# Optimization experiments

Measured on AMD Instinct MI355X. Metric: run time of the kernel, lower is better.

Reference implementation:

```python
import jax, jax.numpy as jnp
import numpy as np

N, E = 100000, 1600000
IN_C, HID, OUT_C = 128, 16, 32
H1, H2 = 8, 8  # heads for conv1/conv2; conv3 has 1 head, concat=False
NEG_SLOPE = 0.2


def setup_inputs() -> dict:
    key = jax.random.key(0)
    ks = jax.random.split(key, 16)
    def p(k, shape, fan_in):
        return jax.random.normal(k, shape, jnp.float32) * (1.0 / np.sqrt(fan_in))
    inp = {
        "x": jax.random.normal(ks[0], (N, IN_C), jnp.float32),
        "edge_index": jax.random.randint(ks[1], (2, E), 0, N, jnp.int32),
        # conv1: in=128 -> heads=8, ch=16, concat
        "W1": p(ks[2], (IN_C, H1 * HID), IN_C),
        "a_src1": p(ks[3], (H1, HID), HID),
        "a_dst1": p(ks[4], (H1, HID), HID),
        "b1": jnp.zeros((H1 * HID,), jnp.float32),
        # conv2: in=128 -> heads=8, ch=16, concat
        "W2": p(ks[5], (H1 * HID, H2 * HID), H1 * HID),
        "a_src2": p(ks[6], (H2, HID), HID),
        "a_dst2": p(ks[7], (H2, HID), HID),
        "b2": jnp.zeros((H2 * HID,), jnp.float32),
        # conv3: in=128 -> heads=1, ch=32, concat=False
        "W3": p(ks[8], (H2 * HID, OUT_C), H2 * HID),
        "a_src3": p(ks[9], (1, OUT_C), OUT_C),
        "a_dst3": p(ks[10], (1, OUT_C), OUT_C),
        "b3": jnp.zeros((OUT_C,), jnp.float32),
    }
    return inp


def gat_conv(x, src, dst, W, a_src, a_dst, b, heads, ch, concat):
    """PyG-style GATConv (eval mode): gather -> leaky_relu -> segment softmax -> scatter sum."""
    n = x.shape[0]
    h = (x @ W).reshape(n, heads, ch)                 # [N, H, C]
    al_s = jnp.sum(h * a_src, axis=-1)                # [N, H] source-side logit part
    al_d = jnp.sum(h * a_dst, axis=-1)                # [N, H] dest-side logit part
    logits = jax.nn.leaky_relu(al_s[src] + al_d[dst], NEG_SLOPE)  # [Etot, H]
    m = jax.ops.segment_max(logits, dst, num_segments=n)         # per-dest max (self loops guarantee >=1 edge)
    e = jnp.exp(logits - m[dst])
    denom = jax.ops.segment_sum(e, dst, num_segments=n)
    alpha = e / denom[dst]                            # [Etot, H]
    msgs = h[src] * alpha[..., None]                  # [Etot, H, C]
    out = jax.ops.segment_sum(msgs, dst, num_segments=n)  # [N, H, C]
    if concat:
        return out.reshape(n, heads * ch) + b
    return out.mean(axis=1) + b


def reference(x, edge_index, W1, a_src1, a_dst1, b1, W2, a_src2, a_dst2, b2,
              W3, a_src3, a_dst3, b3):
    n = x.shape[0]
    loops = jnp.arange(n, dtype=edge_index.dtype)     # PyG add_self_loops=True
    src = jnp.concatenate([edge_index[0], loops])
    dst = jnp.concatenate([edge_index[1], loops])
    h = jax.nn.relu(gat_conv(x, src, dst, W1, a_src1, a_dst1, b1, H1, HID, True))
    h = jax.nn.relu(gat_conv(h, src, dst, W2, a_src2, a_dst2, b2, H2, HID, True))
    h = gat_conv(h, src, dst, W3, a_src3, a_dst3, b3, 1, OUT_C, False)
    # global_mean_pool with all-zero batch vector -> mean over all nodes
    return h.mean(axis=0, keepdims=True)              # [1, OUT_C]
```

## Files before the change

kernel.cpp:

```cpp
#include <hip/hip_runtime.h>


typedef unsigned short bfu;
typedef unsigned char u8;
typedef __attribute__((ext_vector_type(8))) short bf16x8;
typedef __attribute__((ext_vector_type(4))) float f32x4;
typedef __attribute__((ext_vector_type(2))) float f32x2;

constexpr int N_NODES = 100000;
constexpr int E_IN    = 1600000;
constexpr int E_TOT   = E_IN + N_NODES;
constexpr float NEG   = 0.2f;
constexpr int P_XCD   = 8;
constexpr int PSZ     = N_NODES / P_XCD;
constexpr int CAP     = 64;
constexpr int AGG32_B = N_NODES / 32;
constexpr int AGG128_B = N_NODES / 32;
constexpr int GEMM_B  = (N_NODES + 63) / 64;
constexpr int EDGE_B4 = (E_TOT / 4 + 255) / 256;
constexpr int FILL_B  = EDGE_B4 * P_XCD;
constexpr int PREP_ITEMS = 43008;
constexpr int PREP_B  = (PREP_ITEMS + 255) / 256;

__device__ inline bfu f2bf(float f) {
    union { float f; unsigned i; } c; c.f = f;
    unsigned x = c.i;
    return (bfu)((x + 0x7fffu + ((x >> 16) & 1u)) >> 16);
}
__device__ inline u8 f2fp8(float f) {
    return (u8)(__builtin_amdgcn_cvt_pk_fp8_f32(f, f, 0, false) & 0xff);
}


__device__ inline void prep_body(int idx,
        const float* __restrict__ W1, const float* __restrict__ W2,
        const float* __restrict__ W3,
        const float* __restrict__ as1, const float* __restrict__ ad1,
        const float* __restrict__ as2, const float* __restrict__ ad2,
        const float* __restrict__ as3, const float* __restrict__ ad3,
        bfu* __restrict__ WtX1, bfu* __restrict__ WtX2, bfu* __restrict__ WtX3) {
    if (idx < 16384) {
        int k = idx >> 7, n = idx & 127;
        WtX1[n * 128 + k] = f2bf(W1[idx]);
    } else if (idx < 32768) {
        int r = idx - 16384;
        int k = r >> 7, n = r & 127;
        WtX2[n * 128 + k] = f2bf(W2[r]);
    } else if (idx < 36864) {
        int r = idx - 32768;
        int k = r >> 5, n = r & 31;
        WtX3[n * 128 + k] = f2bf(W3[r]);
    } else if (idx < 38912) {
        int r = idx - 36864;
        int sd = r >> 10, rr = r & 1023;
        int h = rr >> 7, k = rr & 127;
        const float* a = sd ? ad1 : as1;
        float v = 0.f;
        #pragma unroll
        for (int c = 0; c < 16; ++c) v += W1[k * 128 + h * 16 + c] * a[h * 16 + c];
        WtX1[(128 + sd * 8 + h) * 128 + k] = f2bf(v);
    } else if (idx < 40960) {
        int r = idx - 38912;
        int sd = r >> 10, rr = r & 1023;
        int h = rr >> 7, k = rr & 127;
        const float* a = sd ? ad2 : as2;
        float v = 0.f;
        #pragma unroll
        for (int c = 0; c < 16; ++c) v += W2[k * 128 + h * 16 + c] * a[h * 16 + c];
        WtX2[(128 + sd * 8 + h) * 128 + k] = f2bf(v);
    } else if (idx < 41216) {
        int r = idx - 40960;
        int sd = r >> 7, k = r & 127;
        const float* a = sd ? ad3 : as3;
        float v = 0.f;
        #pragma unroll
        for (int c = 0; c < 32; ++c) v += W3[k * 32 + c] * a[c];
        WtX3[(32 + sd) * 128 + k] = f2bf(v);
    } else if (idx < 43008) {
        WtX3[34 * 128 + (idx - 41216)] = 0;
    }
}


__global__ __launch_bounds__(256) void fill_prep(const int* __restrict__ ei,
        int* __restrict__ cursor, int* __restrict__ srclist,
        const float* __restrict__ W1, const float* __restrict__ W2,
        const float* __restrict__ W3,
        const float* __restrict__ as1, const float* __restrict__ ad1,
        const float* __restrict__ as2, const float* __restrict__ ad2,
        const float* __restrict__ as3, const float* __restrict__ ad3,
        bfu* __restrict__ WtX1, bfu* __restrict__ WtX2, bfu* __restrict__ WtX3) {
    if (blockIdx.x >= FILL_B) {
        int idx = (blockIdx.x - FILL_B) * 256 + threadIdx.x;
        prep_body(idx, W1, W2, W3, as1, ad1, as2, ad2, as3, ad3, WtX1, WtX2, WtX3);
        return;
    }
    int p = blockIdx.x & 7;
    int b = blockIdx.x >> 3;
    int lo = p * PSZ, hi = lo + PSZ;
    int e0 = (b * 256 + threadIdx.x) * 4;
    if (e0 >= E_TOT) return;
    bool self = e0 >= E_IN;
    int4 d4;
    if (!self) d4 = *(const int4*)&ei[E_IN + e0];
    else { int bb = e0 - E_IN; d4 = make_int4(bb, bb + 1, bb + 2, bb + 3); }
    int dd[4] = {d4.x, d4.y, d4.z, d4.w};
    #pragma unroll
    for (int q = 0; q < 4; ++q) {
        int d = dd[q];
        if (d >= lo && d < hi) {
            int s = self ? (e0 - E_IN + q) : ei[e0 + q];
            int pos = atomicAdd(&cursor[d], 1);
            if (pos < CAP) srclist[d * CAP + pos] = s;
        }
    }
}


__device__ inline bf16x8 ldcvt_f32(const float* p) {
    float4 v0 = *(const float4*)p;
    float4 v1 = *(const float4*)(p + 4);
    bf16x8 a;
    a[0] = (short)f2bf(v0.x); a[1] = (short)f2bf(v0.y);
    a[2] = (short)f2bf(v0.z); a[3] = (short)f2bf(v0.w);
    a[4] = (short)f2bf(v1.x); a[5] = (short)f2bf(v1.y);
    a[6] = (short)f2bf(v1.z); a[7] = (short)f2bf(v1.w);
    return a;
}

template<int NTO, bool F32A>
__global__ __launch_bounds__(256) void gemm_mfma(const void* __restrict__ Xg_,
                                                 const bfu* __restrict__ Wt,
                                                 u8* __restrict__ Y,
                                                 float* __restrict__ als,
                                                 float* __restrict__ ald) {
    constexpr int COUT = NTO * 16;
    int wid  = threadIdx.x >> 6;
    int lane = threadIdx.x & 63;
    int m = lane & 15, quad = lane >> 4;
    int rbase = (blockIdx.x * 4 + wid) * 16;
    if (rbase >= N_NODES) return;
    int rA = rbase + m; if (rA >= N_NODES) rA = N_NODES - 1;

    bf16x8 a0, a1, a2, a3;
    if constexpr (F32A) {
        const float* Ap = (const float*)Xg_ + (size_t)rA * 128 + quad * 8;
        a0 = ldcvt_f32(Ap);
        a1 = ldcvt_f32(Ap + 32);
        a2 = ldcvt_f32(Ap + 64);
        a3 = ldcvt_f32(Ap + 96);
    } else {
        const bfu* Ap = (const bfu*)Xg_ + (size_t)rA * 128 + quad * 8;
        a0 = *(const bf16x8*)(Ap);
        a1 = *(const bf16x8*)(Ap + 32);
        a2 = *(const bf16x8*)(Ap + 64);
        a3 = *(const bf16x8*)(Ap + 96);
    }

    const bfu* Bp = Wt + (size_t)m * 128 + quad * 8;
    f32x4 acc[NTO + 1];
    #pragma unroll
    for (int nt = 0; nt <= NTO; nt++) {
        const bfu* Bn = Bp + nt * 16 * 128;
        f32x4 c = {0.f, 0.f, 0.f, 0.f};
        c = __builtin_amdgcn_mfma_f32_16x16x32_bf16(a0, *(const bf16x8*)(Bn),      c, 0, 0, 0);
        c = __builtin_amdgcn_mfma_f32_16x16x32_bf16(a1, *(const bf16x8*)(Bn + 32), c, 0, 0, 0);
        c = __builtin_amdgcn_mfma_f32_16x16x32_bf16(a2, *(const bf16x8*)(Bn + 64), c, 0, 0, 0);
        c = __builtin_amdgcn_mfma_f32_16x16x32_bf16(a3, *(const bf16x8*)(Bn + 96), c, 0, 0, 0);
        acc[nt] = c;
    }

    #pragma unroll
    for (int nt = 0; nt < NTO; nt++) {
        #pragma unroll
        for (int r = 0; r < 4; r++) {
            int row = rbase + quad * 4 + r;
            if (row < N_NODES)
                Y[(size_t)row * COUT + nt * 16 + m] = f2fp8(acc[nt][r]);
        }
    }
    #pragma unroll
    for (int r = 0; r < 4; r++) {
        int row = rbase + quad * 4 + r;
        if (row >= N_NODES) continue;
        float v = acc[NTO][r];
        if constexpr (NTO == 8) {
            if (m < 8) als[row * 8 + m] = v;
            else       ald[row * 8 + (m - 8)] = v;
        } else {
            if (m == 0) als[row] = v;
            else if (m == 1) ald[row] = v;
        }
    }
}


__device__ inline void unpack_fma(uint4 u, float w, float* a) {
    f32x2 p;
    p = __builtin_amdgcn_cvt_pk_f32_fp8((int)u.x, false); a[0]=fmaf(w,p[0],a[0]);  a[1]=fmaf(w,p[1],a[1]);
    p = __builtin_amdgcn_cvt_pk_f32_fp8((int)u.x, true);  a[2]=fmaf(w,p[0],a[2]);  a[3]=fmaf(w,p[1],a[3]);
    p = __builtin_amdgcn_cvt_pk_f32_fp8((int)u.y, false); a[4]=fmaf(w,p[0],a[4]);  a[5]=fmaf(w,p[1],a[5]);
    p = __builtin_amdgcn_cvt_pk_f32_fp8((int)u.y, true);  a[6]=fmaf(w,p[0],a[6]);  a[7]=fmaf(w,p[1],a[7]);
    p = __builtin_amdgcn_cvt_pk_f32_fp8((int)u.z, false); a[8]=fmaf(w,p[0],a[8]);  a[9]=fmaf(w,p[1],a[9]);
    p = __builtin_amdgcn_cvt_pk_f32_fp8((int)u.z, true);  a[10]=fmaf(w,p[0],a[10]); a[11]=fmaf(w,p[1],a[11]);
    p = __builtin_amdgcn_cvt_pk_f32_fp8((int)u.w, false); a[12]=fmaf(w,p[0],a[12]); a[13]=fmaf(w,p[1],a[13]);
    p = __builtin_amdgcn_cvt_pk_f32_fp8((int)u.w, true);  a[14]=fmaf(w,p[0],a[14]); a[15]=fmaf(w,p[1],a[15]);
}

__global__ __launch_bounds__(256) void agg128(const u8* __restrict__ Hb,
        const float* __restrict__ als, const float* __restrict__ ald,
        const int* __restrict__ deg, const int* __restrict__ srclist,
        const float* __restrict__ bias, bfu* __restrict__ out) {
    int wave = blockIdx.x * 4 + (threadIdx.x >> 6);
    int lane = threadIdx.x & 63;
    int sub  = lane >> 3;
    int li   = lane & 7;
    int d    = wave * 8 + sub;
    int c0   = li * 16;
    float ad = ald[d * 8 + li];
    const int* sl = srclist + d * CAP;
    int n = deg[d]; n = n < CAP ? n : CAP;
    float a[16];
    #pragma unroll
    for (int k = 0; k < 16; ++k) a[k] = 0.f;
    float den = 0.f;
    int j = 0;
    for (; j + 2 <= n; j += 2) {
        int s0 = sl[j], s1 = sl[j + 1];
        uint4 u0 = *(const uint4*)(Hb + (size_t)s0 * 128 + c0);
        uint4 u1 = *(const uint4*)(Hb + (size_t)s1 * 128 + c0);
        float x0 = als[s0 * 8 + li], x1 = als[s1 * 8 + li];
        float l0 = x0 + ad; l0 = fmaxf(l0, NEG * l0); float w0 = __expf(l0);
        float l1 = x1 + ad; l1 = fmaxf(l1, NEG * l1); float w1 = __expf(l1);
        den += w0 + w1;
        unpack_fma(u0, w0, a);
        unpack_fma(u1, w1, a);
    }
    if (j < n) {
        int s0 = sl[j];
        uint4 u0 = *(const uint4*)(Hb + (size_t)s0 * 128 + c0);
        float x0 = als[s0 * 8 + li];
        float l0 = x0 + ad; l0 = fmaxf(l0, NEG * l0); float w0 = __expf(l0);
        den += w0;
        unpack_fma(u0, w0, a);
    }
    float r = 1.f / den;
    unsigned dw[8];
    #pragma unroll
    for (int k = 0; k < 8; ++k) {
        float e0 = fmaxf(fmaf(a[2*k],   r, bias[c0 + 2*k]),   0.f);
        float e1 = fmaxf(fmaf(a[2*k+1], r, bias[c0 + 2*k+1]), 0.f);
        dw[k] = (unsigned)f2bf(e0) | ((unsigned)f2bf(e1) << 16);
    }
    uint4 st0 = {dw[0], dw[1], dw[2], dw[3]};
    uint4 st1 = {dw[4], dw[5], dw[6], dw[7]};
    *(uint4*)&out[(size_t)d * 128 + c0]     = st0;
    *(uint4*)&out[(size_t)d * 128 + c0 + 8] = st1;
}

__global__ __launch_bounds__(256) void agg32(const u8* __restrict__ Hb,
        const float* __restrict__ als, const float* __restrict__ ald,
        const int* __restrict__ deg, const int* __restrict__ srclist,
        const float* __restrict__ bias, float* __restrict__ outp) {
    __shared__ float lds[4][32];
    int t    = threadIdx.x;
    int wid  = t >> 6;
    int lane = t & 63;
    int sub  = lane >> 3;
    int li   = lane & 7;
    int d    = blockIdx.x * 32 + wid * 8 + sub;
    int c0 = li * 4;
    float adv = ald[d];
    const int* sl = srclist + d * CAP;
    int n = deg[d]; n = n < CAP ? n : CAP;
    float a0=0.f,a1=0.f,a2=0.f,a3=0.f,den=0.f;
    int j = 0;
    for (; j + 4 <= n; j += 4) {
        int s0 = sl[j], s1 = sl[j+1], s2 = sl[j+2], s3 = sl[j+3];
        unsigned u0 = *(const unsigned*)(Hb + (size_t)s0 * 32 + c0);
        unsigned u1 = *(const unsigned*)(Hb + (size_t)s1 * 32 + c0);
        unsigned u2 = *(const unsigned*)(Hb + (size_t)s2 * 32 + c0);
        unsigned u3 = *(const unsigned*)(Hb + (size_t)s3 * 32 + c0);
        float x0 = als[s0], x1 = als[s1], x2 = als[s2], x3 = als[s3];
        float l0 = x0 + adv; l0 = fmaxf(l0, NEG*l0); float w0 = __expf(l0);
        float l1 = x1 + adv; l1 = fmaxf(l1, NEG*l1); float w1 = __expf(l1);
        float l2 = x2 + adv; l2 = fmaxf(l2, NEG*l2); float w2 = __expf(l2);
        float l3 = x3 + adv; l3 = fmaxf(l3, NEG*l3); float w3 = __expf(l3);
        den += (w0 + w1) + (w2 + w3);
        f32x2 p;
        p = __builtin_amdgcn_cvt_pk_f32_fp8((int)u0, false); a0=fmaf(w0,p[0],a0); a1=fmaf(w0,p[1],a1);
        p = __builtin_amdgcn_cvt_pk_f32_fp8((int)u0, true);  a2=fmaf(w0,p[0],a2); a3=fmaf(w0,p[1],a3);
        p = __builtin_amdgcn_cvt_pk_f32_fp8((int)u1, false); a0=fmaf(w1,p[0],a0); a1=fmaf(w1,p[1],a1);
        p = __builtin_amdgcn_cvt_pk_f32_fp8((int)u1, true);  a2=fmaf(w1,p[0],a2); a3=fmaf(w1,p[1],a3);
        p = __builtin_amdgcn_cvt_pk_f32_fp8((int)u2, false); a0=fmaf(w2,p[0],a0); a1=fmaf(w2,p[1],a1);
        p = __builtin_amdgcn_cvt_pk_f32_fp8((int)u2, true);  a2=fmaf(w2,p[0],a2); a3=fmaf(w2,p[1],a3);
        p = __builtin_amdgcn_cvt_pk_f32_fp8((int)u3, false); a0=fmaf(w3,p[0],a0); a1=fmaf(w3,p[1],a1);
        p = __builtin_amdgcn_cvt_pk_f32_fp8((int)u3, true);  a2=fmaf(w3,p[0],a2); a3=fmaf(w3,p[1],a3);
    }
    for (; j < n; ++j) {
        int s0 = sl[j];
        unsigned u0 = *(const unsigned*)(Hb + (size_t)s0 * 32 + c0);
        float x0 = als[s0];
        float l0 = x0 + adv; l0 = fmaxf(l0, NEG*l0); float w0 = __expf(l0);
        den += w0;
        f32x2 p;
        p = __builtin_amdgcn_cvt_pk_f32_fp8((int)u0, false); a0=fmaf(w0,p[0],a0); a1=fmaf(w0,p[1],a1);
        p = __builtin_amdgcn_cvt_pk_f32_fp8((int)u0, true);  a2=fmaf(w0,p[0],a2); a3=fmaf(w0,p[1],a3);
    }
    float r = 1.f / den;
    float4 bv = *(const float4*)&bias[c0];
    float o0 = fmaf(a0, r, bv.x), o1 = fmaf(a1, r, bv.y);
    float o2 = fmaf(a2, r, bv.z), o3 = fmaf(a3, r, bv.w);
    #pragma unroll
    for (int mask = 8; mask < 64; mask <<= 1) {
        o0 += __shfl_xor(o0, mask);
        o1 += __shfl_xor(o1, mask);
        o2 += __shfl_xor(o2, mask);
        o3 += __shfl_xor(o3, mask);
    }
    if (sub == 0) {
        lds[wid][c0]     = o0;
        lds[wid][c0 + 1] = o1;
        lds[wid][c0 + 2] = o2;
        lds[wid][c0 + 3] = o3;
    }
    __syncthreads();
    if (t < 32)
        atomicAdd(&outp[t],
            (lds[0][t] + lds[1][t] + lds[2][t] + lds[3][t]) * (1.0f / N_NODES));
}


extern "C" void kernel_launch(void* const* d_in, const int* in_sizes, int n_in,
                              void* d_out, int out_size, void* d_ws, size_t ws_size,
                              hipStream_t stream) {
    (void)in_sizes; (void)n_in; (void)out_size; (void)ws_size;
    const float* x   = (const float*)d_in[0];
    const int*   ei  = (const int*)d_in[1];
    const float* W1  = (const float*)d_in[2];
    const float* as1 = (const float*)d_in[3];
    const float* ad1 = (const float*)d_in[4];
    const float* b1  = (const float*)d_in[5];
    const float* W2  = (const float*)d_in[6];
    const float* as2 = (const float*)d_in[7];
    const float* ad2 = (const float*)d_in[8];
    const float* b2  = (const float*)d_in[9];
    const float* W3  = (const float*)d_in[10];
    const float* as3 = (const float*)d_in[11];
    const float* ad3 = (const float*)d_in[12];
    const float* b3  = (const float*)d_in[13];

    char* ws = (char*)d_ws;
    size_t off = 0;
    auto carve = [&](size_t bytes) { void* p = ws + off; off += (bytes + 255) & ~size_t(255); return p; };
    u8*    bufH    = (u8*)carve(size_t(N_NODES) * 128);
    bfu*   bufF    = (bfu*)carve(size_t(N_NODES) * 128 * 2);
    float* als     = (float*)carve(size_t(N_NODES) * 8 * 4);
    float* ald     = (float*)carve(size_t(N_NODES) * 8 * 4);
    int*   cursor  = (int*)carve(size_t(N_NODES) * 4);
    bfu*   WtX1    = (bfu*)carve(144 * 128 * 2);
    bfu*   WtX2    = (bfu*)carve(144 * 128 * 2);
    bfu*   WtX3    = (bfu*)carve(48 * 128 * 2);
    int*   srclist = (int*)carve(size_t(N_NODES) * CAP * 4);

    hipMemsetAsync(cursor, 0, size_t(N_NODES) * 4, stream);
    hipMemsetAsync(d_out, 0, 32 * 4, stream);

    fill_prep<<<FILL_B + PREP_B, 256, 0, stream>>>(ei, cursor, srclist,
        W1, W2, W3, as1, ad1, as2, ad2, as3, ad3, WtX1, WtX2, WtX3);

    gemm_mfma<8, true><<<GEMM_B, 256, 0, stream>>>(x, WtX1, bufH, als, ald);
    agg128<<<AGG128_B, 256, 0, stream>>>(bufH, als, ald, cursor, srclist, b1, bufF);

    gemm_mfma<8, false><<<GEMM_B, 256, 0, stream>>>(bufF, WtX2, bufH, als, ald);
    agg128<<<AGG128_B, 256, 0, stream>>>(bufH, als, ald, cursor, srclist, b2, bufF);

    gemm_mfma<2, false><<<GEMM_B, 256, 0, stream>>>(bufF, WtX3, bufH, als, ald);
    agg32<<<AGG32_B, 256, 0, stream>>>(bufH, als, ald, cursor, srclist, b3, (float*)d_out);
}
```

Baseline: 438.3 us.

## Merge edge-bucket fill with layer-1 GEMM and fold memsets into prep kernel

Splits weight prep into its own small kernel, which also zeroes the cursor array and the output, replacing the two memset calls. The CSR-style edge fill and the first-layer MFMA GEMM now run in one interleaved grid (64 fill blocks per 8 GEMM blocks), so the atomic-heavy fill and the compute-bound GEMM can overlap instead of running back to back. Streaming loads of the edge index and x use nontemporal hints to reduce cache pollution. The cost is an extra prep launch before the merged grid and the occupancy hint of 5 waves-per-SIMD on the merged kernel.

```diff
diff --git a/kernel.cpp b/kernel.cpp
--- a/kernel.cpp
+++ b/kernel.cpp
@@ -6,6 +6,8 @@
 typedef __attribute__((ext_vector_type(8))) short bf16x8;
 typedef __attribute__((ext_vector_type(4))) float f32x4;
 typedef __attribute__((ext_vector_type(2))) float f32x2;
+typedef __attribute__((ext_vector_type(4))) int i32x4;
+typedef __attribute__((ext_vector_type(4))) float fx4;
 
 constexpr int N_NODES = 100000;
 constexpr int E_IN    = 1600000;
@@ -21,6 +23,10 @@
 constexpr int FILL_B  = EDGE_B4 * P_XCD;
 constexpr int PREP_ITEMS = 43008;
 constexpr int PREP_B  = (PREP_ITEMS + 255) / 256;
+
+constexpr int FG_GRID = ((FILL_B - 1) / 64) * 72 + ((FILL_B - 1) % 64) + 1;
+static_assert(((GEMM_B - 1) / 8) * 72 + 64 + ((GEMM_B - 1) % 8) < FG_GRID,
+              "gemm blocks must fit inside merged grid");
 
 __device__ inline bfu f2bf(float f) {
     union { float f; unsigned i; } c; c.f = f;
@@ -81,35 +87,37 @@
     }
 }
 
-
-__global__ __launch_bounds__(256) void fill_prep(const int* __restrict__ ei,
-        int* __restrict__ cursor, int* __restrict__ srclist,
+__global__ __launch_bounds__(256) void prep_cursor(
         const float* __restrict__ W1, const float* __restrict__ W2,
         const float* __restrict__ W3,
         const float* __restrict__ as1, const float* __restrict__ ad1,
         const float* __restrict__ as2, const float* __restrict__ ad2,
         const float* __restrict__ as3, const float* __restrict__ ad3,
-        bfu* __restrict__ WtX1, bfu* __restrict__ WtX2, bfu* __restrict__ WtX3) {
-    if (blockIdx.x >= FILL_B) {
-        int idx = (blockIdx.x - FILL_B) * 256 + threadIdx.x;
-        prep_body(idx, W1, W2, W3, as1, ad1, as2, ad2, as3, ad3, WtX1, WtX2, WtX3);
-        return;
-    }
-    int p = blockIdx.x & 7;
-    int b = blockIdx.x >> 3;
+        bfu* __restrict__ WtX1, bfu* __restrict__ WtX2, bfu* __restrict__ WtX3,
+        int* __restrict__ cursor, float* __restrict__ outp) {
+    int idx = blockIdx.x * 256 + threadIdx.x;
+    prep_body(idx, W1, W2, W3, as1, ad1, as2, ad2, as3, ad3, WtX1, WtX2, WtX3);
+    for (int i = idx; i < N_NODES; i += PREP_ITEMS) cursor[i] = 0;
+    if (idx < 32) outp[idx] = 0.f;
+}
+
+
+__device__ inline void fill_body(int fb, const int* __restrict__ ei,
+        int* __restrict__ cursor, int* __restrict__ srclist) {
+    int p = fb & 7;
+    int b = fb >> 3;
     int lo = p * PSZ, hi = lo + PSZ;
     int e0 = (b * 256 + threadIdx.x) * 4;
     if (e0 >= E_TOT) return;
     bool self = e0 >= E_IN;
-    int4 d4;
-    if (!self) d4 = *(const int4*)&ei[E_IN + e0];
-    else { int bb = e0 - E_IN; d4 = make_int4(bb, bb + 1, bb + 2, bb + 3); }
-    int dd[4] = {d4.x, d4.y, d4.z, d4.w};
+    i32x4 d4;
+    if (!self) d4 = __builtin_nontemporal_load((const i32x4*)&ei[E_IN + e0]);
+    else { int bb = e0 - E_IN; d4[0] = bb; d4[1] = bb + 1; d4[2] = bb + 2; d4[3] = bb + 3; }
     #pragma unroll
     for (int q = 0; q < 4; ++q) {
-        int d = dd[q];
+        int d = d4[q];
         if (d >= lo && d < hi) {
-            int s = self ? (e0 - E_IN + q) : ei[e0 + q];
+            int s = self ? (e0 - E_IN + q) : __builtin_nontemporal_load(&ei[e0 + q]);
             int pos = atomicAdd(&cursor[d], 1);
             if (pos < CAP) srclist[d * CAP + pos] = s;
         }
@@ -117,38 +125,38 @@
 }
 
 
-__device__ inline bf16x8 ldcvt_f32(const float* p) {
-    float4 v0 = *(const float4*)p;
-    float4 v1 = *(const float4*)(p + 4);
+__device__ inline bf16x8 ldcvt_f32_nt(const float* p) {
+    fx4 v0 = __builtin_nontemporal_load((const fx4*)p);
+    fx4 v1 = __builtin_nontemporal_load((const fx4*)(p + 4));
     bf16x8 a;
-    a[0] = (short)f2bf(v0.x); a[1] = (short)f2bf(v0.y);
-    a[2] = (short)f2bf(v0.z); a[3] = (short)f2bf(v0.w);
-    a[4] = (short)f2bf(v1.x); a[5] = (short)f2bf(v1.y);
-    a[6] = (short)f2bf(v1.z); a[7] = (short)f2bf(v1.w);
+    a[0] = (short)f2bf(v0[0]); a[1] = (short)f2bf(v0[1]);
+    a[2] = (short)f2bf(v0[2]); a[3] = (short)f2bf(v0[3]);
+    a[4] = (short)f2bf(v1[0]); a[5] = (short)f2bf(v1[1]);
+    a[6] = (short)f2bf(v1[2]); a[7] = (short)f2bf(v1[3]);
     return a;
 }
 
 template<int NTO, bool F32A>
-__global__ __launch_bounds__(256) void gemm_mfma(const void* __restrict__ Xg_,
-                                                 const bfu* __restrict__ Wt,
-                                                 u8* __restrict__ Y,
-                                                 float* __restrict__ als,
-                                                 float* __restrict__ ald) {
+__device__ inline void gemm_body(int bid, const void* __restrict__ Xg_,
+                                 const bfu* __restrict__ Wt,
+                                 u8* __restrict__ Y,
+                                 float* __restrict__ als,
+                                 float* __restrict__ ald) {
     constexpr int COUT = NTO * 16;
     int wid  = threadIdx.x >> 6;
     int lane = threadIdx.x & 63;
     int m = lane & 15, quad = lane >> 4;
-    int rbase = (blockIdx.x * 4 + wid) * 16;
+    int rbase = (bid * 4 + wid) * 16;
     if (rbase >= N_NODES) return;
     int rA = rbase + m; if (rA >= N_NODES) rA = N_NODES - 1;
 
     bf16x8 a0, a1, a2, a3;
     if constexpr (F32A) {
         const float* Ap = (const float*)Xg_ + (size_t)rA * 128 + quad * 8;
-        a0 = ldcvt_f32(Ap);
-        a1 = ldcvt_f32(Ap + 32);
-        a2 = ldcvt_f32(Ap + 64);
-        a3 = ldcvt_f32(Ap + 96);
+        a0 = ldcvt_f32_nt(Ap);
+        a1 = ldcvt_f32_nt(Ap + 32);
+        a2 = ldcvt_f32_nt(Ap + 64);
+        a3 = ldcvt_f32_nt(Ap + 96);
     } else {
         const bfu* Ap = (const bfu*)Xg_ + (size_t)rA * 128 + quad * 8;
         a0 = *(const bf16x8*)(Ap);
@@ -191,6 +199,34 @@
             if (m == 0) als[row] = v;
             else if (m == 1) ald[row] = v;
         }
+    }
+}
+
+template<int NTO, bool F32A>
+__global__ __launch_bounds__(256) void gemm_mfma(const void* __restrict__ Xg_,
+                                                 const bfu* __restrict__ Wt,
+                                                 u8* __restrict__ Y,
+                                                 float* __restrict__ als,
+                                                 float* __restrict__ ald) {
+    gemm_body<NTO, F32A>(blockIdx.x, Xg_, Wt, Y, als, ald);
+}
+
+
+__global__ __launch_bounds__(256, 5) void fill_gemm1(
+        const int* __restrict__ ei, int* __restrict__ cursor,
+        int* __restrict__ srclist,
+        const float* __restrict__ x, const bfu* __restrict__ WtX1,
+        u8* __restrict__ Y, float* __restrict__ als, float* __restrict__ ald) {
+    int bid = blockIdx.x;
+    int grp = bid / 72, rem = bid % 72;
+    if (rem < 64) {
+        int fb = grp * 64 + rem;
+        if (fb >= FILL_B) return;
+        fill_body(fb, ei, cursor, srclist);
+    } else {
+        int gb = grp * 8 + (rem - 64);
+        if (gb >= GEMM_B) return;
+        gemm_body<8, true>(gb, x, WtX1, Y, als, ald);
     }
 }
 
@@ -363,13 +399,12 @@
     bfu*   WtX3    = (bfu*)carve(48 * 128 * 2);
     int*   srclist = (int*)carve(size_t(N_NODES) * CAP * 4);
 
-    hipMemsetAsync(cursor, 0, size_t(N_NODES) * 4, stream);
-    hipMemsetAsync(d_out, 0, 32 * 4, stream);
-
-    fill_prep<<<FILL_B + PREP_B, 256, 0, stream>>>(ei, cursor, srclist,
-        W1, W2, W3, as1, ad1, as2, ad2, as3, ad3, WtX1, WtX2, WtX3);
-
-    gemm_mfma<8, true><<<GEMM_B, 256, 0, stream>>>(x, WtX1, bufH, als, ald);
+    prep_cursor<<<PREP_B, 256, 0, stream>>>(W1, W2, W3,
+        as1, ad1, as2, ad2, as3, ad3, WtX1, WtX2, WtX3, cursor, (float*)d_out);
+
+    fill_gemm1<<<FG_GRID, 256, 0, stream>>>(ei, cursor, srclist,
+        x, WtX1, bufH, als, ald);
+
     agg128<<<AGG128_B, 256, 0, stream>>>(bufH, als, ald, cursor, srclist, b1, bufF);
 
     gemm_mfma<8, false><<<GEMM_B, 256, 0, stream>>>(bufF, WtX2, bufH, als, ald);
```

New measurement: 444.5 us. Within noise of the previous version (+1.4%).
